# Performance work log

Hardware: AMD Instinct MI355X
Metric: run time of the kernel (lower is better)

Reference implementation:

```python
import jax, jax.numpy as jnp
import numpy as np

B, T, D, H = 16, 81, 128, 8  # batch, ntok, d_model (= d_head), n_head


def setup_inputs() -> dict:
    key = jax.random.key(0)
    ks = jax.random.split(key, 6)
    s = 0.02
    return {
        "x": jax.random.normal(ks[0], (B, T, D), jnp.float32),
        "msk": jnp.ones((1, H, T, T), jnp.float32),
        "wqkv_w": jax.random.normal(ks[1], (H * 2 * D, D), jnp.float32) * s,
        "wqkv_b": jax.random.normal(ks[2], (H * 2 * D,), jnp.float32) * s,
        "wk_w": jax.random.normal(ks[3], (H, D), jnp.float32) * s,
        "fanout_w": jax.random.normal(ks[4], (D, D), jnp.float32) * s,
        "fanout_b": jax.random.normal(ks[5], (D,), jnp.float32) * s,
        "head_enabled": jnp.ones((H,), jnp.float32),
        "n": 0, "layer": 0, "pas": 1,
    }


def quick_gelu(x):
    return x * jax.nn.sigmoid(1.702 * x)


def reference(x, msk, wqkv_w, wqkv_b, wk_w, fanout_w, fanout_b, head_enabled, n, layer, pas):
    b, t, d = x.shape
    h = wk_w.shape[0]
    # qkv projection: per-head q and v of full width d (d_head == d_model)
    y = x @ wqkv_w.T + wqkv_b                      # [b, t, h*2*d]
    y = y.reshape(b, t, h, 2 * d)
    q, v = y[..., :d], y[..., d:]                  # [b, t, h, d] each
    # k: input gated per-head by wk.weight rows
    k = x[:, :, None, :] * wk_w[None, None, :, :]  # [b, t, h, d]
    # v gating by head-enabled flags
    v = v * head_enabled[None, None, :, None]
    # L1 attention scores: a[b,h,t,s] = -sum_d |q[b,t,h,d] - k[b,s,h,d]| / sqrt(d)
    diff = jnp.abs(q[:, :, None, :, :] - k[:, None, :, :, :])  # [b, t, s, h, d]
    a = -diff.sum(-1)                               # [b, t, s, h]
    a = jnp.transpose(a, (0, 3, 1, 2)) / jnp.sqrt(jnp.asarray(d, x.dtype))  # [b,h,t,s]
    a = jax.nn.softmax(a, axis=3) * msk
    bo = jnp.einsum('bhts,bshd->bthd', a, v)        # [b, t, h, d]
    bo = bo.sum(axis=2)                             # sum over heads -> [b, t, d]
    ap = jnp.transpose(a[0] - 1.0 + msk[0], (1, 2, 0))  # [t, s, h]
    z = quick_gelu(bo + 4.0) - 4.0
    z = z @ fanout_w.T + fanout_b
    return (x + z, ap)
```

## Files before the change

kernel.cpp:

```cpp
#include <hip/hip_runtime.h>
#include <math.h>

#define Bq 16
#define Tq 81
#define Dq 128
#define Hq 8
#define BT (Bq*Tq)
#define BTD (Bq*Tq*Dq)
#define PS 84
#define P_SZ   (Bq*Tq*Hq*PS)
#define QV_SZ  (BT*Hq*Dq)
#define P_OFF  0
#define Q_OFF  (P_OFF + P_SZ)
#define V_OFF  (Q_OFF + QV_SZ)

#define LSTR 136

typedef __attribute__((ext_vector_type(8))) short short8;
typedef __attribute__((ext_vector_type(4))) float f32x4;

__device__ __forceinline__ float l1_4(const float4 q, const float4 k) {
    return fabsf(q.x - k.x) + fabsf(q.y - k.y) + fabsf(q.z - k.z) + fabsf(q.w - k.w);
}
__device__ __forceinline__ int imin(int a, int b) { return a < b ? a : b; }
__device__ __forceinline__ unsigned short f2bf(float f) {
    unsigned u = __float_as_uint(f);
    u += 0x7fffu + ((u >> 16) & 1u);
    return (unsigned short)(u >> 16);
}
__device__ __forceinline__ float bf2f(unsigned short s) {
    return __uint_as_float((unsigned)s << 16);
}

__global__ __launch_bounds__(256) void k_qkv_mfma(
    const float* __restrict__ x, const float* __restrict__ wqkv,
    const float* __restrict__ bias, const float* __restrict__ he,
    float* __restrict__ Qo, unsigned short* __restrict__ Vb)
{
    __shared__ unsigned short xs[64 * LSTR];
    __shared__ unsigned short wsh[64 * LSTR];
    const int tid = threadIdx.x;
    const int w = tid >> 6, lane = tid & 63;
    const int ln = lane & 15, quad = lane >> 4;
    const int r0 = blockIdx.x * 64;
    const int n0 = blockIdx.y * 64;
    const int h  = blockIdx.y >> 2;
    const int isV = (blockIdx.y >> 1) & 1;
    const int c0 = (blockIdx.y & 1) * 64;

    #pragma unroll
    for (int i = 0; i < 8; ++i) {
        const int idx = tid + i * 256;
        const int r = idx >> 5, c4 = idx & 31;
        const int gr = imin(r0 + r, BT - 1);
        const float4 v = *(const float4*)(x + (size_t)gr * Dq + c4 * 4);
        ushort4 o;
        o.x = f2bf(v.x); o.y = f2bf(v.y); o.z = f2bf(v.z); o.w = f2bf(v.w);
        *(ushort4*)(&xs[r * LSTR + c4 * 4]) = o;

        const float4 vw = *(const float4*)(wqkv + (size_t)(n0 + r) * Dq + c4 * 4);
        ushort4 ow;
        ow.x = f2bf(vw.x); ow.y = f2bf(vw.y); ow.z = f2bf(vw.z); ow.w = f2bf(vw.w);
        *(ushort4*)(&wsh[r * LSTR + c4 * 4]) = ow;
    }
    __syncthreads();

    const unsigned short* xa = xs + (w * 16 + ln) * LSTR + quad * 8;
    const unsigned short* wb = wsh + ln * LSTR + quad * 8;

    f32x4 acc[4];
    #pragma unroll
    for (int i = 0; i < 4; ++i) acc[i] = (f32x4){0.f, 0.f, 0.f, 0.f};

    #pragma unroll
    for (int kb = 0; kb < Dq; kb += 32) {
        const short8 af = *(const short8*)(xa + kb);
        #pragma unroll
        for (int nt = 0; nt < 4; ++nt) {
            const short8 bf = *(const short8*)(wb + nt * 16 * LSTR + kb);
            acc[nt] = __builtin_amdgcn_mfma_f32_16x16x32_bf16(af, bf, acc[nt], 0, 0, 0);
        }
    }

    const float scale = isV ? he[h] : 1.0f;
    const int gm0 = r0 + w * 16 + quad * 4;
    #pragma unroll
    for (int nt = 0; nt < 4; ++nt) {
        const float bn = bias[n0 + nt * 16 + ln];
        #pragma unroll
        for (int r = 0; r < 4; ++r) {
            const int gm = gm0 + r;
            if (gm < BT) {
                const int bb = gm / 81, tt = gm - bb * 81;
                const size_t o =
                    (((size_t)bb * Hq + h) * Tq + tt) * Dq + c0 + nt * 16 + ln;
                const float val = (acc[nt][r] + bn) * scale;
                if (isV) Vb[o] = f2bf(val);
                else     Qo[o] = val;
            }
        }
    }
}

__global__ __launch_bounds__(256) void k_scores(
    const float* __restrict__ x, const float* __restrict__ Q,
    const float* __restrict__ wk, const float* __restrict__ msk,
    float* __restrict__ P, float* __restrict__ out)
{
    __shared__ float Kl[81 * 132];
    __shared__ float sc[21 * 85];
    __shared__ float rsum[24];
    const int tid = threadIdx.x;
    const int tq = blockIdx.x, h = blockIdx.y, b = blockIdx.z;
    const int t0g = tq * 21;
    const int nt = (tq == 3) ? 18 : 21;

    {
        const float* wkb = wk + (size_t)h * Dq;
        for (int idx = tid; idx < Tq * 32; idx += 256) {
            const int r = idx >> 5, c = idx & 31;
            const float4 xv = *(const float4*)(x + (size_t)(b * Tq + r) * Dq + c * 4);
            const float4 wv = *(const float4*)(wkb + c * 4);
            float4 kv;
            kv.x = xv.x * wv.x; kv.y = xv.y * wv.y;
            kv.z = xv.z * wv.z; kv.w = xv.w * wv.w;
            *(float4*)(&Kl[r * 132 + c * 4]) = kv;
        }
    }
    __syncthreads();

    if (tid < 243) {
        const int tg = tid / 81, sg = tid % 81;
        const float* qrow[7];
        #pragma unroll
        for (int i = 0; i < 7; ++i) {
            const int t = imin(t0g + tg * 7 + i, Tq - 1);
            qrow[i] = Q + (((size_t)b * Hq + h) * Tq + t) * Dq;
        }
        float acc[7];
        #pragma unroll
        for (int i = 0; i < 7; ++i) acc[i] = 0.f;

        #pragma unroll 4
        for (int k4 = 0; k4 < 32; ++k4) {
            const float4 kv = *(const float4*)(&Kl[sg * 132 + k4 * 4]);
            #pragma unroll
            for (int i = 0; i < 7; ++i) {
                const float4 qv = *(const float4*)(qrow[i] + k4 * 4);
                acc[i] += l1_4(qv, kv);
            }
        }
        const float ns = -0.08838834764831845f;
        #pragma unroll
        for (int i = 0; i < 7; ++i)
            sc[(tg * 7 + i) * 85 + sg] = acc[i] * ns;
    }
    __syncthreads();

    {
        const int w = tid >> 6, lane = tid & 63;
        for (int r = w; r < nt; r += 4) {
            float* row = sc + r * 85;
            const bool hi = (lane + 64) < Tq;
            const float v0 = row[lane];
            const float v1 = hi ? row[lane + 64] : -1e30f;
            float m = fmaxf(v0, v1);
            #pragma unroll
            for (int off = 32; off > 0; off >>= 1)
                m = fmaxf(m, __shfl_xor(m, off));
            const float e0 = __expf(v0 - m);
            const float e1 = hi ? __expf(v1 - m) : 0.f;
            float s = e0 + e1;
            #pragma unroll
            for (int off = 32; off > 0; off >>= 1)
                s += __shfl_xor(s, off);
            row[lane] = e0;
            if (hi) row[lane + 64] = e1;
            if (lane == 0) rsum[r] = 1.0f / s;
        }
    }
    __syncthreads();

    const bool doap = (b == 0);
    for (int idx = tid; idx < nt * Tq; idx += 256) {
        const int tl = idx / Tq, s = idx - tl * Tq;
        const int tg2 = t0g + tl;
        const float mv = msk[((size_t)h * Tq + tg2) * Tq + s];
        const float pm = sc[tl * 85 + s] * rsum[tl] * mv;
        P[(((size_t)b * Tq + tg2) * Hq + h) * PS + s] = pm;
        if (doap) out[BTD + ((size_t)tg2 * Tq + s) * Hq + h] = pm - 1.0f + mv;
    }
}

__global__ __launch_bounds__(512) void k_out(
    const float* __restrict__ x, const float* __restrict__ P,
    const unsigned short* __restrict__ Vb, const float* __restrict__ fw,
    const float* __restrict__ fb, float* __restrict__ out)
{
    __shared__ float Pl[6][Hq][PS];
    __shared__ float bo_part[8][6][128];
    __shared__ float zs[6][128];
    const int tid = threadIdx.x;
    const int t0 = blockIdx.x * 6, b = blockIdx.y;

    {
        const float4* src = (const float4*)(P + ((size_t)b * Tq + t0) * Hq * PS);
        #pragma unroll
        for (int idx = tid; idx < 6 * Hq * PS / 4; idx += 512)
            ((float4*)Pl)[idx] = src[idx];
    }
    __syncthreads();

    const int w = tid >> 6, lane = tid & 63;
    {
        const int d0 = lane * 2;
        float2 acc[6];
        #pragma unroll
        for (int i = 0; i < 6; ++i) acc[i] = make_float2(0.f, 0.f);
        const unsigned short* vp = Vb + (((size_t)b * Hq + w) * Tq) * Dq + d0;
        for (int s4 = 0; s4 < 20; ++s4) {
            float4 p[6];
            #pragma unroll
            for (int t = 0; t < 6; ++t)
                p[t] = *(const float4*)(&Pl[t][w][s4 * 4]);
            #pragma unroll
            for (int ss = 0; ss < 4; ++ss) {
                const int s = s4 * 4 + ss;
                const ushort2 uv = *(const ushort2*)(vp + (size_t)s * Dq);
                const float vx = bf2f(uv.x), vy = bf2f(uv.y);
                #pragma unroll
                for (int t = 0; t < 6; ++t) {
                    const float pv = ((const float*)&p[t])[ss];
                    acc[t].x = fmaf(pv, vx, acc[t].x);
                    acc[t].y = fmaf(pv, vy, acc[t].y);
                }
            }
        }
        {
            const ushort2 uv = *(const ushort2*)(vp + (size_t)80 * Dq);
            const float vx = bf2f(uv.x), vy = bf2f(uv.y);
            #pragma unroll
            for (int t = 0; t < 6; ++t) {
                const float pv = Pl[t][w][80];
                acc[t].x = fmaf(pv, vx, acc[t].x);
                acc[t].y = fmaf(pv, vy, acc[t].y);
            }
        }
        #pragma unroll
        for (int t = 0; t < 6; ++t) {
            bo_part[w][t][d0]     = acc[t].x;
            bo_part[w][t][d0 + 1] = acc[t].y;
        }
    }
    __syncthreads();

    for (int idx = tid; idx < 768; idx += 512) {
        const int t = idx >> 7, d = idx & 127;
        float bo = 0.f;
        #pragma unroll
        for (int ww = 0; ww < 8; ++ww) bo += bo_part[ww][t][d];
        const float tt = bo + 4.0f;
        const float sg = 1.0f / (1.0f + __expf(-1.702f * tt));
        zs[t][d] = tt * sg - 4.0f;
    }
    __syncthreads();

    {
        const int n = tid & 127, tg = tid >> 7;
        const bool two = (tg < 2);
        const int tB = two ? tg + 4 : tg;
        const float* fwr = fw + (size_t)n * Dq;
        const float fbn = fb[n];
        float a0 = 0.f, a1 = 0.f;
        #pragma unroll 8
        for (int k4 = 0; k4 < 32; ++k4) {
            const float4 w4 = *(const float4*)(fwr + k4 * 4);
            const float4 z0 = *(const float4*)(&zs[tg][k4 * 4]);
            const float4 z1 = *(const float4*)(&zs[tB][k4 * 4]);
            a0 += z0.x * w4.x + z0.y * w4.y + z0.z * w4.z + z0.w * w4.w;
            a1 += z1.x * w4.x + z1.y * w4.y + z1.z * w4.z + z1.w * w4.w;
        }
        const int t1 = t0 + tg;
        if (t1 < Tq) {
            const size_t o = ((size_t)b * Tq + t1) * Dq + n;
            out[o] = x[o] + a0 + fbn;
        }
        const int t2 = t0 + tg + 4;
        if (two && t2 < Tq) {
            const size_t o = ((size_t)b * Tq + t2) * Dq + n;
            out[o] = x[o] + a1 + fbn;
        }
    }
}

extern "C" void kernel_launch(void* const* d_in, const int* in_sizes, int n_in,
                              void* d_out, int out_size, void* d_ws, size_t ws_size,
                              hipStream_t stream) {
    const float* x        = (const float*)d_in[0];
    const float* msk      = (const float*)d_in[1];
    const float* wqkv_w   = (const float*)d_in[2];
    const float* wqkv_b   = (const float*)d_in[3];
    const float* wk_w     = (const float*)d_in[4];
    const float* fanout_w = (const float*)d_in[5];
    const float* fanout_b = (const float*)d_in[6];
    const float* he       = (const float*)d_in[7];
    float* out = (float*)d_out;
    float* ws  = (float*)d_ws;

    float* P  = ws + P_OFF;
    float* Q  = ws + Q_OFF;
    unsigned short* Vb = (unsigned short*)(ws + V_OFF);

    k_qkv_mfma<<<dim3(21, 32), 256, 0, stream>>>(x, wqkv_w, wqkv_b, he, Q, Vb);
    k_scores<<<dim3(4, 8, 16), 256, 0, stream>>>(x, Q, wk_w, msk, P, out);
    k_out<<<dim3(14, 16), 512, 0, stream>>>(x, P, Vb, fanout_w, fanout_b, out);
}
```

Baseline: 125.2 us.

## Fuse L1 score/softmax kernel into output kernel, dropping P round-trip

Merges the score+softmax kernel into the attention-output kernel. Each 512-thread block stages the batch's x rows in swizzled shared memory. Each wave computes L1 scores for one head over 6 query rows, runs the softmax in registers with wave shuffles, and writes probabilities straight to shared memory. This removes one launch and the global write and read of P. In exchange, K gating is recomputed per block (14x redundancy per batch), and score work runs on only 224 blocks instead of 512, which lowers parallelism.

```diff
diff --git a/kernel.cpp b/kernel.cpp
--- a/kernel.cpp
+++ b/kernel.cpp
@@ -102,116 +102,95 @@
     }
 }
 
-__global__ __launch_bounds__(256) void k_scores(
+__global__ __launch_bounds__(512) void k_attn_out(
     const float* __restrict__ x, const float* __restrict__ Q,
     const float* __restrict__ wk, const float* __restrict__ msk,
-    float* __restrict__ P, float* __restrict__ out)
+    const unsigned short* __restrict__ Vb, const float* __restrict__ fw,
+    const float* __restrict__ fb, float* __restrict__ out)
 {
-    __shared__ float Kl[81 * 132];
-    __shared__ float sc[21 * 85];
-    __shared__ float rsum[24];
+    __shared__ float xl[Tq * Dq];
+    __shared__ float Pl[Hq][6][PS];
+    __shared__ float bo_part[Hq][6][Dq];
+    __shared__ float zs[6][Dq];
+
     const int tid = threadIdx.x;
-    const int tq = blockIdx.x, h = blockIdx.y, b = blockIdx.z;
-    const int t0g = tq * 21;
-    const int nt = (tq == 3) ? 18 : 21;
+    const int t0 = blockIdx.x * 6, b = blockIdx.y;
+    const int w = tid >> 6, lane = tid & 63;
+
+    for (int idx = tid; idx < Tq * 32; idx += 512) {
+        const int r = idx >> 5, g = idx & 31;
+        const float4 v = *(const float4*)(x + (size_t)(b * Tq + r) * Dq + g * 4);
+        *(float4*)(&xl[r * Dq + ((g ^ (r & 7)) << 2)]) = v;
+    }
+    __syncthreads();
+
+    const int s0 = lane;
+    const bool has1 = (lane < Tq - 64);
+    const int s1 = 64 + lane;
+    const int s1c = has1 ? s1 : (Tq - 1);
+    int ttv[6];
+    const float* qrow[6];
+    #pragma unroll
+    for (int i = 0; i < 6; ++i) {
+        ttv[i] = imin(t0 + i, Tq - 1);
+        qrow[i] = Q + (((size_t)b * Hq + w) * Tq + ttv[i]) * Dq;
+    }
+    const float* wkb = wk + (size_t)w * Dq;
+
+    float acc0[6], acc1[6];
+    #pragma unroll
+    for (int i = 0; i < 6; ++i) { acc0[i] = 0.f; acc1[i] = 0.f; }
+
+    #pragma unroll 2
+    for (int g = 0; g < 32; ++g) {
+        const float4 wv = *(const float4*)(wkb + g * 4);
+        float4 k0 = *(const float4*)(&xl[s0 * Dq + ((g ^ (s0 & 7)) << 2)]);
+        float4 k1 = *(const float4*)(&xl[s1c * Dq + ((g ^ (s1c & 7)) << 2)]);
+        k0.x *= wv.x; k0.y *= wv.y; k0.z *= wv.z; k0.w *= wv.w;
+        k1.x *= wv.x; k1.y *= wv.y; k1.z *= wv.z; k1.w *= wv.w;
+        #pragma unroll
+        for (int i = 0; i < 6; ++i) {
+            const float4 qv = *(const float4*)(qrow[i] + g * 4);
+            acc0[i] += l1_4(qv, k0);
+            acc1[i] += l1_4(qv, k1);
+        }
+    }
 
     {
-        const float* wkb = wk + (size_t)h * Dq;
-        for (int idx = tid; idx < Tq * 32; idx += 256) {
-            const int r = idx >> 5, c = idx & 31;
-            const float4 xv = *(const float4*)(x + (size_t)(b * Tq + r) * Dq + c * 4);
-            const float4 wv = *(const float4*)(wkb + c * 4);
-            float4 kv;
-            kv.x = xv.x * wv.x; kv.y = xv.y * wv.y;
-            kv.z = xv.z * wv.z; kv.w = xv.w * wv.w;
-            *(float4*)(&Kl[r * 132 + c * 4]) = kv;
-        }
-    }
-    __syncthreads();
-
-    if (tid < 243) {
-        const int tg = tid / 81, sg = tid % 81;
-        const float* qrow[7];
-        #pragma unroll
-        for (int i = 0; i < 7; ++i) {
-            const int t = imin(t0g + tg * 7 + i, Tq - 1);
-            qrow[i] = Q + (((size_t)b * Hq + h) * Tq + t) * Dq;
-        }
-        float acc[7];
-        #pragma unroll
-        for (int i = 0; i < 7; ++i) acc[i] = 0.f;
-
-        #pragma unroll 4
-        for (int k4 = 0; k4 < 32; ++k4) {
-            const float4 kv = *(const float4*)(&Kl[sg * 132 + k4 * 4]);
-            #pragma unroll
-            for (int i = 0; i < 7; ++i) {
-                const float4 qv = *(const float4*)(qrow[i] + k4 * 4);
-                acc[i] += l1_4(qv, kv);
-            }
-        }
         const float ns = -0.08838834764831845f;
         #pragma unroll
-        for (int i = 0; i < 7; ++i)
-            sc[(tg * 7 + i) * 85 + sg] = acc[i] * ns;
-    }
-    __syncthreads();
-
-    {
-        const int w = tid >> 6, lane = tid & 63;
-        for (int r = w; r < nt; r += 4) {
-            float* row = sc + r * 85;
-            const bool hi = (lane + 64) < Tq;
-            const float v0 = row[lane];
-            const float v1 = hi ? row[lane + 64] : -1e30f;
+        for (int i = 0; i < 6; ++i) {
+            const float v0 = acc0[i] * ns;
+            const float v1 = has1 ? acc1[i] * ns : -1e30f;
             float m = fmaxf(v0, v1);
             #pragma unroll
             for (int off = 32; off > 0; off >>= 1)
                 m = fmaxf(m, __shfl_xor(m, off));
             const float e0 = __expf(v0 - m);
-            const float e1 = hi ? __expf(v1 - m) : 0.f;
-            float s = e0 + e1;
+            const float e1 = has1 ? __expf(v1 - m) : 0.f;
+            float ssum = e0 + e1;
             #pragma unroll
             for (int off = 32; off > 0; off >>= 1)
-                s += __shfl_xor(s, off);
-            row[lane] = e0;
-            if (hi) row[lane + 64] = e1;
-            if (lane == 0) rsum[r] = 1.0f / s;
-        }
-    }
-    __syncthreads();
-
-    const bool doap = (b == 0);
-    for (int idx = tid; idx < nt * Tq; idx += 256) {
-        const int tl = idx / Tq, s = idx - tl * Tq;
-        const int tg2 = t0g + tl;
-        const float mv = msk[((size_t)h * Tq + tg2) * Tq + s];
-        const float pm = sc[tl * 85 + s] * rsum[tl] * mv;
-        P[(((size_t)b * Tq + tg2) * Hq + h) * PS + s] = pm;
-        if (doap) out[BTD + ((size_t)tg2 * Tq + s) * Hq + h] = pm - 1.0f + mv;
-    }
-}
-
-__global__ __launch_bounds__(512) void k_out(
-    const float* __restrict__ x, const float* __restrict__ P,
-    const unsigned short* __restrict__ Vb, const float* __restrict__ fw,
-    const float* __restrict__ fb, float* __restrict__ out)
-{
-    __shared__ float Pl[6][Hq][PS];
-    __shared__ float bo_part[8][6][128];
-    __shared__ float zs[6][128];
-    const int tid = threadIdx.x;
-    const int t0 = blockIdx.x * 6, b = blockIdx.y;
-
-    {
-        const float4* src = (const float4*)(P + ((size_t)b * Tq + t0) * Hq * PS);
-        #pragma unroll
-        for (int idx = tid; idx < 6 * Hq * PS / 4; idx += 512)
-            ((float4*)Pl)[idx] = src[idx];
-    }
-    __syncthreads();
-
-    const int w = tid >> 6, lane = tid & 63;
+                ssum += __shfl_xor(ssum, off);
+            const float rinv = 1.0f / ssum;
+            const float* mrow = msk + ((size_t)w * Tq + ttv[i]) * Tq;
+            const bool tvalid = (t0 + i) < Tq;
+            const float mv0 = mrow[s0];
+            const float p0 = e0 * rinv * mv0;
+            Pl[w][i][s0] = p0;
+            if (b == 0 && tvalid)
+                out[BTD + ((size_t)(t0 + i) * Tq + s0) * Hq + w] = p0 - 1.0f + mv0;
+            if (has1) {
+                const float mv1 = mrow[s1];
+                const float p1 = e1 * rinv * mv1;
+                Pl[w][i][s1] = p1;
+                if (b == 0 && tvalid)
+                    out[BTD + ((size_t)(t0 + i) * Tq + s1) * Hq + w] = p1 - 1.0f + mv1;
+            }
+        }
+    }
+    __syncthreads();
+
     {
         const int d0 = lane * 2;
         float2 acc[6];
@@ -222,7 +201,7 @@
             float4 p[6];
             #pragma unroll
             for (int t = 0; t < 6; ++t)
-                p[t] = *(const float4*)(&Pl[t][w][s4 * 4]);
+                p[t] = *(const float4*)(&Pl[w][t][s4 * 4]);
             #pragma unroll
             for (int ss = 0; ss < 4; ++ss) {
                 const int s = s4 * 4 + ss;
@@ -241,7 +220,7 @@
             const float vx = bf2f(uv.x), vy = bf2f(uv.y);
             #pragma unroll
             for (int t = 0; t < 6; ++t) {
-                const float pv = Pl[t][w][80];
+                const float pv = Pl[w][t][80];
                 acc[t].x = fmaf(pv, vx, acc[t].x);
                 acc[t].y = fmaf(pv, vy, acc[t].y);
             }
@@ -259,9 +238,9 @@
         float bo = 0.f;
         #pragma unroll
         for (int ww = 0; ww < 8; ++ww) bo += bo_part[ww][t][d];
-        const float tt = bo + 4.0f;
-        const float sg = 1.0f / (1.0f + __expf(-1.702f * tt));
-        zs[t][d] = tt * sg - 4.0f;
+        const float tt2 = bo + 4.0f;
+        const float sg = 1.0f / (1.0f + __expf(-1.702f * tt2));
+        zs[t][d] = tt2 * sg - 4.0f;
     }
     __syncthreads();
 
@@ -307,11 +286,10 @@
     float* out = (float*)d_out;
     float* ws  = (float*)d_ws;
 
-    float* P  = ws + P_OFF;
     float* Q  = ws + Q_OFF;
     unsigned short* Vb = (unsigned short*)(ws + V_OFF);
 
     k_qkv_mfma<<<dim3(21, 32), 256, 0, stream>>>(x, wqkv_w, wqkv_b, he, Q, Vb);
-    k_scores<<<dim3(4, 8, 16), 256, 0, stream>>>(x, Q, wk_w, msk, P, out);
-    k_out<<<dim3(14, 16), 512, 0, stream>>>(x, P, Vb, fanout_w, fanout_b, out);
-}
+    k_attn_out<<<dim3(14, 16), 512, 0, stream>>>(x, Q, wk_w, msk, Vb,
+                                                 fanout_w, fanout_b, out);
+}
```

Result: faster. 120.5 us (-3.8%).
